# Performance work log

Measured on AMD Instinct MI355X. Metric: run time of the kernel, lower is better.

Reference implementation:

```python
import jax, jax.numpy as jnp
import numpy as np

B, S, D, H = 2, 2048, 1024, 16
DK = D // H


def setup_inputs() -> dict:
    key = jax.random.key(0)
    ks = jax.random.split(key, 7)
    q = jax.random.normal(ks[0], (B, S, D), dtype=jnp.float32)
    k = jax.random.normal(ks[1], (B, S, D), dtype=jnp.float32)
    v = jax.random.normal(ks[2], (B, S, D), dtype=jnp.float32)
    # causal mask: mask==0 positions get -1e9 before softmax
    mask = jnp.tril(jnp.ones((S, S), dtype=jnp.int32))[None, None, :, :]
    scale = 0.02
    w_q = jax.random.normal(ks[3], (D, D), dtype=jnp.float32) * scale
    w_k = jax.random.normal(ks[4], (D, D), dtype=jnp.float32) * scale
    w_v = jax.random.normal(ks[5], (D, D), dtype=jnp.float32) * scale
    w_o = jax.random.normal(ks[6], (D, D), dtype=jnp.float32) * scale
    return {"q": q, "k": k, "v": v, "mask": mask,
            "w_q": w_q, "w_k": w_k, "w_v": w_v, "w_o": w_o}


def reference(q, k, v, mask, w_q, w_k, w_v, w_o):
    # nn.Linear(bias=False): x @ W.T
    query = q @ w_q.T  # [B,S,D]
    key = k @ w_k.T
    value = v @ w_v.T
    # split heads -> [B,H,S,DK]
    query = query.reshape(B, S, H, DK).transpose(0, 2, 1, 3)
    key = key.reshape(B, S, H, DK).transpose(0, 2, 1, 3)
    value = value.reshape(B, S, H, DK).transpose(0, 2, 1, 3)
    scores = jnp.einsum('bhqd,bhkd->bhqk', query, key) / jnp.sqrt(
        jnp.asarray(DK, dtype=query.dtype))
    scores = jnp.where(mask == 0, jnp.asarray(-1e9, scores.dtype), scores)
    attn = jax.nn.softmax(scores, axis=-1)  # dropout p=0.0 -> identity
    x = jnp.einsum('bhqk,bhkd->bhqd', attn, value)  # [B,H,S,DK]
    x = x.transpose(0, 2, 1, 3).reshape(B, S, D)
    return x @ w_o.T
```

## Files before the change

kernel.cpp:

```cpp
#include <hip/hip_runtime.h>

typedef __attribute__((ext_vector_type(8))) short short8;
typedef __attribute__((ext_vector_type(4))) float f32x4;

#define DEVI static __device__ __forceinline__

constexpr int BB = 2, SS = 2048, DD = 1024, HH = 16, DKK = 64;
constexpr size_t QN = (size_t)BB * SS * DD;
constexpr size_t WN = (size_t)DD * DD;

constexpr size_t OFF_WQ = 3 * QN;
constexpr size_t OFF_WO = OFF_WQ + 3 * WN;
constexpr size_t OFF_QM = OFF_WQ + 4 * WN;
constexpr size_t OFF_KM = OFF_QM + QN;
constexpr size_t OFF_VM = OFF_QM + 2 * QN;
constexpr size_t OFF_XC = OFF_QM + 3 * QN;

DEVI unsigned short f2bf(float f) {
  unsigned int u = __float_as_uint(f);
  u = (u + 0x7fffu + ((u >> 16) & 1u)) >> 16;
  return (unsigned short)u;
}

DEVI f32x4 fzero() { f32x4 z = {0.f, 0.f, 0.f, 0.f}; return z; }

DEVI void gld16(const void* g, void* l) {
  __builtin_amdgcn_global_load_lds((__attribute__((address_space(1))) void*)g,
                                   (__attribute__((address_space(3))) void*)l,
                                   16, 0, 0);
}

DEVI short8 mk8u(unsigned int a, unsigned int b, unsigned int c, unsigned int d) {
  union { short8 s; unsigned int u[4]; } x;
  x.u[0] = a; x.u[1] = b; x.u[2] = c; x.u[3] = d;
  return x.s;
}

DEVI short8 mk8q(unsigned long long lo, unsigned long long hi) {
  union { short8 s; unsigned long long q[2]; } x;
  x.q[0] = lo; x.q[1] = hi;
  return x.s;
}

DEVI unsigned int pkbf(float a, float b) {
  return __builtin_amdgcn_perm(__float_as_uint(b), __float_as_uint(a), 0x07060302u);
}

#define VMBAR(N) asm volatile("s_waitcnt vmcnt(" #N ")\n\ts_barrier" ::: "memory")
#define LGKM0                                      \
  do {                                             \
    asm volatile("s_waitcnt lgkmcnt(0)" ::: "memory"); \
    __builtin_amdgcn_sched_barrier(0);             \
  } while (0)

__global__ __launch_bounds__(256) void convert_all(
    const float* __restrict__ q, const float* __restrict__ k,
    const float* __restrict__ v, const float* __restrict__ wq,
    const float* __restrict__ wk, const float* __restrict__ wv,
    const float* __restrict__ wo, unsigned short* __restrict__ ws) {
  size_t t = (size_t)blockIdx.x * 256 + threadIdx.x;
  size_t e = t * 4;
  const float* src;
  size_t base, idx;
  if (e < 3 * QN) {
    size_t a = e >> 22;
    idx = e & (QN - 1);
    src = (a == 0) ? q : (a == 1) ? k : v;
    base = a * QN;
  } else {
    size_t r = e - 3 * QN;
    size_t a = r >> 20;
    idx = r & (WN - 1);
    src = (a == 0) ? wq : (a == 1) ? wk : (a == 2) ? wv : wo;
    base = 3 * QN + a * WN;
  }
  float4 f = *(const float4*)(src + idx);
  ushort4 o;
  o.x = f2bf(f.x); o.y = f2bf(f.y); o.z = f2bf(f.z); o.w = f2bf(f.w);
  *(ushort4*)(ws + base + idx) = o;
}

__global__ __launch_bounds__(512, 2) void proj_gemm(unsigned short* __restrict__ ws) {
  __shared__ unsigned short lds[65536];
  const int tid = threadIdx.x;
  const int w = tid >> 6, l = tid & 63;
  const int lr = l & 15, qd = l >> 4, l7 = l & 7, l3 = l >> 3;
  const int wr = w >> 2, wc = w & 3;

  const int orig = blockIdx.x;
  const int swz = (orig & 7) * 24 + (orig >> 3);
  const int mt = swz >> 2, nt = swz & 3;
  const int z = mt >> 4;
  const int m0 = (mt & 15) * 256, n0 = nt * 256;

  const unsigned short* Ab = ws + (size_t)z * QN;
  const unsigned short* Wb = ws + OFF_WQ + (size_t)z * WN;
  unsigned short* O = ws + OFF_QM + (size_t)z * QN;

  f32x4 acc[8][4];
#pragma unroll
  for (int i = 0; i < 8; ++i)
#pragma unroll
    for (int j = 0; j < 4; ++j) acc[i][j] = fzero();

  auto stage = [&](int buf, int ab, int h, int kt) {
    const unsigned short* src = ab ? Wb : Ab;
    const int rc0 = (ab ? n0 : m0) + h * 128 + w * 8 + l3;
    const int kofs = kt * 64 + ((l7 ^ l3) * 8);
    unsigned short* d = &lds[buf * 32768 + ab * 16384 + h * 8192 + w * 512];
#pragma unroll
    for (int u = 0; u < 2; ++u)
      gld16(src + (size_t)(rc0 + u * 64) * DD + kofs, d + u * 4096);
  };
  auto rdA = [&](int buf, int fi, int ks) -> short8 {
    const int rg = (fi * 2 + wr) * 16 + lr;
    const int c2 = (ks * 4 + qd) ^ l7;
    return *(const short8*)&lds[buf * 32768 + rg * 64 + c2 * 8];
  };
  auto rdB = [&](int buf, int fj, int ks) -> short8 {
    const int rg = (fj * 4 + wc) * 16 + lr;
    const int c2 = (ks * 4 + qd) ^ l7;
    return *(const short8*)&lds[buf * 32768 + 16384 + rg * 64 + c2 * 8];
  };

  stage(0, 0, 0, 0);
  stage(0, 1, 0, 0);
  stage(0, 1, 1, 0);
  stage(0, 0, 1, 0);

  constexpr int NT = DD / 64;
#pragma unroll 1
  for (int t = 0; t < NT; ++t) {
    const int rb = t & 1, wb = rb ^ 1;
    const bool g = (t + 1 < NT);
    short8 af[4][2], bf[2][2], bh[2][2];

    VMBAR(4);
    if (g) stage(wb, 0, 0, t + 1);
#pragma unroll
    for (int mi = 0; mi < 4; ++mi)
#pragma unroll
      for (int ks = 0; ks < 2; ++ks) af[mi][ks] = rdA(rb, mi, ks);
#pragma unroll
    for (int nj = 0; nj < 2; ++nj)
#pragma unroll
      for (int ks = 0; ks < 2; ++ks) bf[nj][ks] = rdB(rb, nj, ks);
    LGKM0;
    __builtin_amdgcn_s_setprio(1);
#pragma unroll
    for (int mi = 0; mi < 4; ++mi)
#pragma unroll
      for (int nj = 0; nj < 2; ++nj)
#pragma unroll
        for (int ks = 0; ks < 2; ++ks)
          acc[mi][nj] = __builtin_amdgcn_mfma_f32_16x16x32_bf16(
              af[mi][ks], bf[nj][ks], acc[mi][nj], 0, 0, 0);
    __builtin_amdgcn_s_setprio(0);

    if (g) { VMBAR(4); } else { VMBAR(2); }
    if (g) stage(wb, 1, 0, t + 1);
#pragma unroll
    for (int nj = 0; nj < 2; ++nj)
#pragma unroll
      for (int ks = 0; ks < 2; ++ks) bh[nj][ks] = rdB(rb, 2 + nj, ks);
    LGKM0;
    __builtin_amdgcn_s_setprio(1);
#pragma unroll
    for (int mi = 0; mi < 4; ++mi)
#pragma unroll
      for (int nj = 0; nj < 2; ++nj)
#pragma unroll
        for (int ks = 0; ks < 2; ++ks)
          acc[mi][2 + nj] = __builtin_amdgcn_mfma_f32_16x16x32_bf16(
              af[mi][ks], bh[nj][ks], acc[mi][2 + nj], 0, 0, 0);
    __builtin_amdgcn_s_setprio(0);

    if (g) { VMBAR(4); } else { VMBAR(0); }
    if (g) stage(wb, 1, 1, t + 1);
#pragma unroll
    for (int mi = 0; mi < 4; ++mi)
#pragma unroll
      for (int ks = 0; ks < 2; ++ks) af[mi][ks] = rdA(rb, 4 + mi, ks);
    LGKM0;
    __builtin_amdgcn_s_setprio(1);
#pragma unroll
    for (int mi = 0; mi < 4; ++mi)
#pragma unroll
      for (int nj = 0; nj < 2; ++nj)
#pragma unroll
        for (int ks = 0; ks < 2; ++ks)
          acc[4 + mi][nj] = __builtin_amdgcn_mfma_f32_16x16x32_bf16(
              af[mi][ks], bf[nj][ks], acc[4 + mi][nj], 0, 0, 0);
    __builtin_amdgcn_s_setprio(0);

    if (g) stage(wb, 0, 1, t + 1);
    __builtin_amdgcn_s_setprio(1);
#pragma unroll
    for (int mi = 0; mi < 4; ++mi)
#pragma unroll
      for (int nj = 0; nj < 2; ++nj)
#pragma unroll
        for (int ks = 0; ks < 2; ++ks)
          acc[4 + mi][2 + nj] = __builtin_amdgcn_mfma_f32_16x16x32_bf16(
              af[mi][ks], bh[nj][ks], acc[4 + mi][2 + nj], 0, 0, 0);
    __builtin_amdgcn_s_setprio(0);
  }

  if (z == 2) {
#pragma unroll
    for (int fi = 0; fi < 8; ++fi)
#pragma unroll
      for (int fj = 0; fj < 4; ++fj) {
        const int n = n0 + (fj * 4 + wc) * 16 + lr;
        const int h = n >> 6, dk = n & 63;
        const int m = m0 + (fi * 2 + wr) * 16 + qd * 4;
        const int b = m >> 11, s = m & 2047;
        ushort4 pk;
        pk.x = f2bf(acc[fi][fj][0]); pk.y = f2bf(acc[fi][fj][1]);
        pk.z = f2bf(acc[fi][fj][2]); pk.w = f2bf(acc[fi][fj][3]);
        *(ushort4*)&O[((size_t)(b * HH + h) * DKK + dk) * SS + s] = pk;
      }
  } else {
#pragma unroll
    for (int fi = 0; fi < 8; ++fi)
#pragma unroll
      for (int fj = 0; fj < 4; ++fj) {
        const int n = n0 + (fj * 4 + wc) * 16 + lr;
        const int h = n >> 6, dk = n & 63;
#pragma unroll
        for (int i = 0; i < 4; ++i) {
          const int m = m0 + (fi * 2 + wr) * 16 + qd * 4 + i;
          const int b = m >> 11, s = m & 2047;
          O[((size_t)(b * HH + h) * SS + s) * DKK + dk] = f2bf(acc[fi][fj][i]);
        }
      }
  }
}

__global__ __launch_bounds__(256) void flash_attn(
    const unsigned short* __restrict__ Qm, const unsigned short* __restrict__ Km,
    const unsigned short* __restrict__ Vt, unsigned short* __restrict__ Xc) {
  __shared__ unsigned short Kl[2][4096];
  __shared__ unsigned short Vl[2][4096];
  const int head = blockIdx.x, qy = blockIdx.y, b = blockIdx.z;
  const int qt = (qy < 16) ? qy : 47 - qy;
  const int tid = threadIdx.x, w = tid >> 6, l = tid & 63, lr = l & 15, qd = l >> 4;
  const int slr = lr ^ ((lr >> 3) << 2);
  const size_t bh = (size_t)(b * HH + head);
  const unsigned short* Qb = Qm + bh * SS * DKK;
  const unsigned short* Kb = Km + bh * SS * DKK;
  const unsigned short* Vb = Vt + bh * DKK * SS;

  const int nkv = qt + 1;
  const int qrow = qt * 64 + w * 16 + lr;

  const int s0 = w, s1 = w + 4;
  const unsigned short* kb0 =
      &Kb[(size_t)((s0 >> 1) * 16 + lr) * DKK + (s0 & 1) * 32 + qd * 8];
  const unsigned short* kb1 =
      &Kb[(size_t)((s1 >> 1) * 16 + lr) * DKK + (s1 & 1) * 32 + qd * 8];
  const unsigned short* vb0 =
      &Vb[(size_t)((s0 >> 1) * 16 + slr) * SS + (s0 & 1) * 32 + qd * 8];
  const unsigned short* vb1 =
      &Vb[(size_t)((s1 >> 1) * 16 + slr) * SS + (s1 & 1) * 32 + qd * 8];

  const int loOff = ((qd >> 1) * 16 + slr) * 8 + (qd & 1) * 4;
  const int hiOff = ((2 + (qd >> 1)) * 16 + slr) * 8 + (qd & 1) * 4;

  short8 qf0 = *(const short8*)&Qb[(size_t)qrow * DKK + qd * 8];
  short8 qf1 = *(const short8*)&Qb[(size_t)qrow * DKK + 32 + qd * 8];

  f32x4 o[4];
#pragma unroll
  for (int i = 0; i < 4; ++i) o[i] = fzero();
  float ll = 0.f;
  const float c1 = 0.18033688011112042f;
  const float mc = 8.0f * c1;

  {
    gld16(kb0, &Kl[0][s0 * 512]);
    gld16(kb1, &Kl[0][s1 * 512]);
    gld16(vb0, &Vl[0][s0 * 512]);
    gld16(vb1, &Vl[0][s1 * 512]);
  }

#pragma unroll 1
  for (int kv = 0; kv < nkv; ++kv) {
    __syncthreads();
    const int cur = kv & 1;
    if (kv + 1 < nkv) {
      const size_t koff = (size_t)(kv + 1) * (64 * DKK);
      const size_t voff = (size_t)(kv + 1) * 64;
      gld16(kb0 + koff, &Kl[cur ^ 1][s0 * 512]);
      gld16(kb1 + koff, &Kl[cur ^ 1][s1 * 512]);
      gld16(vb0 + voff, &Vl[cur ^ 1][s0 * 512]);
      gld16(vb1 + voff, &Vl[cur ^ 1][s1 * 512]);
    }

    {
      const int kv0 = kv * 64;
      f32x4 sc[4];
#pragma unroll
      for (int nt = 0; nt < 4; ++nt) {
        short8 kf0 = *(const short8*)&Kl[cur][(nt * 2 + 0) * 512 + l * 8];
        short8 kf1 = *(const short8*)&Kl[cur][(nt * 2 + 1) * 512 + l * 8];
        f32x4 zz = fzero();
        zz = __builtin_amdgcn_mfma_f32_16x16x32_bf16(kf0, qf0, zz, 0, 0, 0);
        sc[nt] = __builtin_amdgcn_mfma_f32_16x16x32_bf16(kf1, qf1, zz, 0, 0, 0);
      }
      if (kv == qt) {
#pragma unroll
        for (int nt = 0; nt < 4; ++nt)
#pragma unroll
          for (int i = 0; i < 4; ++i) {
            const int kvi = kv0 + nt * 16 + qd * 4 + i;
            if (kvi > qrow) sc[nt][i] = -3e38f;
          }
      }

      float rs = 0.f;
#pragma unroll
      for (int nt = 0; nt < 4; ++nt)
#pragma unroll
        for (int i = 0; i < 4; ++i) {
          const float pp = exp2f(fmaf(sc[nt][i], c1, -mc));
          sc[nt][i] = pp;
          rs += pp;
        }
      rs += __shfl_xor(rs, 16);
      rs += __shfl_xor(rs, 32);
      ll += rs;

      unsigned int pd[4][2];
#pragma unroll
      for (int f = 0; f < 4; ++f) {
        pd[f][0] = pkbf(sc[f][0], sc[f][1]);
        pd[f][1] = pkbf(sc[f][2], sc[f][3]);
      }

#pragma unroll
      for (int kh = 0; kh < 2; ++kh) {
        short8 bfr = mk8u(pd[2 * kh][0], pd[2 * kh][1],
                          pd[2 * kh + 1][0], pd[2 * kh + 1][1]);
#pragma unroll
        for (int mt = 0; mt < 4; ++mt) {
          const int sbase = (mt * 2 + kh) * 512;
          const unsigned long long lo =
              *(const unsigned long long*)&Vl[cur][sbase + loOff];
          const unsigned long long hi =
              *(const unsigned long long*)&Vl[cur][sbase + hiOff];
          o[mt] = __builtin_amdgcn_mfma_f32_16x16x32_bf16(mk8q(lo, hi), bfr,
                                                          o[mt], 0, 0, 0);
        }
      }
    }
  }

  const float inv = 1.0f / ll;
  unsigned short* Xr = Xc + ((size_t)b * SS + qrow) * DD + (size_t)head * DKK;
#pragma unroll
  for (int mt = 0; mt < 4; ++mt)
#pragma unroll
    for (int i = 0; i < 4; ++i)
      Xr[mt * 16 + qd * 4 + i] = f2bf(o[mt][i] * inv);
}

__global__ __launch_bounds__(256, 2) void out_gemm(
    const unsigned short* __restrict__ Xc, const unsigned short* __restrict__ Wo,
    float* __restrict__ out) {
  __shared__ unsigned short lds[32768];
  const int tid = threadIdx.x;
  const int w = tid >> 6, l = tid & 63;
  const int lr = l & 15, qd = l >> 4, l7 = l & 7, l3 = l >> 3;
  const int wr = w >> 1, wc = w & 1;
  const int m0 = blockIdx.x * 128, n0 = blockIdx.y * 128;

  f32x4 acc[4][4];
#pragma unroll
  for (int i = 0; i < 4; ++i)
#pragma unroll
    for (int j = 0; j < 4; ++j) acc[i][j] = fzero();

  auto stage = [&](int buf, int ab, int h, int kt) {
    const unsigned short* src = ab ? Wo : Xc;
    const int rc0 = (ab ? n0 : m0) + h * 64 + w * 8 + l3;
    const int kofs = kt * 64 + ((l7 ^ l3) * 8);
    unsigned short* d = &lds[buf * 16384 + ab * 8192 + h * 4096 + w * 512];
#pragma unroll
    for (int u = 0; u < 2; ++u)
      gld16(src + (size_t)(rc0 + u * 32) * DD + kofs, d + u * 2048);
  };
  auto rdA = [&](int buf, int mf, int ks) -> short8 {
    const int rg = mf * 16 + lr;
    const int c2 = (ks * 4 + qd) ^ l7;
    return *(const short8*)&lds[buf * 16384 + rg * 64 + c2 * 8];
  };
  auto rdB = [&](int buf, int nf, int ks) -> short8 {
    const int rg = nf * 16 + lr;
    const int c2 = (ks * 4 + qd) ^ l7;
    return *(const short8*)&lds[buf * 16384 + 8192 + rg * 64 + c2 * 8];
  };

  stage(0, 0, 0, 0);
  stage(0, 1, 0, 0);
  stage(0, 1, 1, 0);
  stage(0, 0, 1, 0);

  constexpr int NT = DD / 64;
#pragma unroll 1
  for (int t = 0; t < NT; ++t) {
    const int rb = t & 1, wb = rb ^ 1;
    const bool g = (t + 1 < NT);
    short8 af[2][2], bf[2][2], bh[2][2];

    VMBAR(4);
    if (g) stage(wb, 0, 0, t + 1);
#pragma unroll
    for (int mi = 0; mi < 2; ++mi)
#pragma unroll
      for (int ks = 0; ks < 2; ++ks) af[mi][ks] = rdA(rb, mi * 2 + wr, ks);
#pragma unroll
    for (int nj = 0; nj < 2; ++nj)
#pragma unroll
      for (int ks = 0; ks < 2; ++ks) bf[nj][ks] = rdB(rb, nj * 2 + wc, ks);
    LGKM0;
    __builtin_amdgcn_s_setprio(1);
#pragma unroll
    for (int mi = 0; mi < 2; ++mi)
#pragma unroll
      for (int nj = 0; nj < 2; ++nj)
#pragma unroll
        for (int ks = 0; ks < 2; ++ks)
          acc[mi][nj] = __builtin_amdgcn_mfma_f32_16x16x32_bf16(
              af[mi][ks], bf[nj][ks], acc[mi][nj], 0, 0, 0);
    __builtin_amdgcn_s_setprio(0);

    if (g) { VMBAR(4); } else { VMBAR(2); }
    if (g) stage(wb, 1, 0, t + 1);
#pragma unroll
    for (int nj = 0; nj < 2; ++nj)
#pragma unroll
      for (int ks = 0; ks < 2; ++ks) bh[nj][ks] = rdB(rb, (2 + nj) * 2 + wc, ks);
    LGKM0;
    __builtin_amdgcn_s_setprio(1);
#pragma unroll
    for (int mi = 0; mi < 2; ++mi)
#pragma unroll
      for (int nj = 0; nj < 2; ++nj)
#pragma unroll
        for (int ks = 0; ks < 2; ++ks)
          acc[mi][2 + nj] = __builtin_amdgcn_mfma_f32_16x16x32_bf16(
              af[mi][ks], bh[nj][ks], acc[mi][2 + nj], 0, 0, 0);
    __builtin_amdgcn_s_setprio(0);

    if (g) { VMBAR(4); } else { VMBAR(0); }
    if (g) stage(wb, 1, 1, t + 1);
#pragma unroll
    for (int mi = 0; mi < 2; ++mi)
#pragma unroll
      for (int ks = 0; ks < 2; ++ks) af[mi][ks] = rdA(rb, (2 + mi) * 2 + wr, ks);
    LGKM0;
    __builtin_amdgcn_s_setprio(1);
#pragma unroll
    for (int mi = 0; mi < 2; ++mi)
#pragma unroll
      for (int nj = 0; nj < 2; ++nj)
#pragma unroll
        for (int ks = 0; ks < 2; ++ks)
          acc[2 + mi][nj] = __builtin_amdgcn_mfma_f32_16x16x32_bf16(
              af[mi][ks], bf[nj][ks], acc[2 + mi][nj], 0, 0, 0);
    __builtin_amdgcn_s_setprio(0);

    if (g) stage(wb, 0, 1, t + 1);
    __builtin_amdgcn_s_setprio(1);
#pragma unroll
    for (int mi = 0; mi < 2; ++mi)
#pragma unroll
      for (int nj = 0; nj < 2; ++nj)
#pragma unroll
        for (int ks = 0; ks < 2; ++ks)
          acc[2 + mi][2 + nj] = __builtin_amdgcn_mfma_f32_16x16x32_bf16(
              af[mi][ks], bh[nj][ks], acc[2 + mi][2 + nj], 0, 0, 0);
    __builtin_amdgcn_s_setprio(0);
  }

#pragma unroll
  for (int a = 0; a < 4; ++a)
#pragma unroll
    for (int c = 0; c < 4; ++c) {
      const int n = n0 + (c * 2 + wc) * 16 + lr;
#pragma unroll
      for (int i = 0; i < 4; ++i) {
        const int m = m0 + (a * 2 + wr) * 16 + qd * 4 + i;
        out[(size_t)m * DD + n] = acc[a][c][i];
      }
    }
}

extern "C" void kernel_launch(void* const* d_in, const int* in_sizes, int n_in,
                              void* d_out, int out_size, void* d_ws, size_t ws_size,
                              hipStream_t stream) {
  (void)in_sizes; (void)n_in; (void)out_size; (void)ws_size;
  const float* q  = (const float*)d_in[0];
  const float* k  = (const float*)d_in[1];
  const float* v  = (const float*)d_in[2];
  const float* wq = (const float*)d_in[4];
  const float* wk = (const float*)d_in[5];
  const float* wv = (const float*)d_in[6];
  const float* wo = (const float*)d_in[7];
  unsigned short* ws = (unsigned short*)d_ws;
  float* out = (float*)d_out;

  convert_all<<<dim3(16384), dim3(256), 0, stream>>>(q, k, v, wq, wk, wv, wo, ws);
  proj_gemm<<<dim3(192), dim3(512), 0, stream>>>(ws);
  flash_attn<<<dim3(16, 32, 2), dim3(256), 0, stream>>>(ws + OFF_QM, ws + OFF_KM,
                                                        ws + OFF_VM, ws + OFF_XC);
  out_gemm<<<dim3(32, 8), dim3(256), 0, stream>>>(ws + OFF_XC, ws + OFF_WO, out);
}
```

Before: 227.6 us.

## Pair heavy and light causal query tiles in one 512-thread attention block

```diff
diff --git a/kernel.cpp b/kernel.cpp
--- a/kernel.cpp
+++ b/kernel.cpp
@@ -237,13 +237,13 @@
   }
 }
 
-__global__ __launch_bounds__(256) void flash_attn(
+__global__ __launch_bounds__(512) void flash_attn(
     const unsigned short* __restrict__ Qm, const unsigned short* __restrict__ Km,
     const unsigned short* __restrict__ Vt, unsigned short* __restrict__ Xc) {
   __shared__ unsigned short Kl[2][4096];
   __shared__ unsigned short Vl[2][4096];
-  const int head = blockIdx.x, qy = blockIdx.y, b = blockIdx.z;
-  const int qt = (qy < 16) ? qy : 47 - qy;
+  const int head = blockIdx.x, py = blockIdx.y, b = blockIdx.z;
+  const int p = b ? 15 - py : py;
   const int tid = threadIdx.x, w = tid >> 6, l = tid & 63, lr = l & 15, qd = l >> 4;
   const int slr = lr ^ ((lr >> 3) << 2);
   const size_t bh = (size_t)(b * HH + head);
@@ -251,19 +251,13 @@
   const unsigned short* Kb = Km + bh * SS * DKK;
   const unsigned short* Vb = Vt + bh * DKK * SS;
 
-  const int nkv = qt + 1;
-  const int qrow = qt * 64 + w * 16 + lr;
-
-  const int s0 = w, s1 = w + 4;
-  const unsigned short* kb0 =
-      &Kb[(size_t)((s0 >> 1) * 16 + lr) * DKK + (s0 & 1) * 32 + qd * 8];
-  const unsigned short* kb1 =
-      &Kb[(size_t)((s1 >> 1) * 16 + lr) * DKK + (s1 & 1) * 32 + qd * 8];
-  const unsigned short* vb0 =
-      &Vb[(size_t)((s0 >> 1) * 16 + slr) * SS + (s0 & 1) * 32 + qd * 8];
-  const unsigned short* vb1 =
-      &Vb[(size_t)((s1 >> 1) * 16 + slr) * SS + (s1 & 1) * 32 + qd * 8];
-
+  const bool heavy = (w < 4);
+  const int qt = heavy ? (31 - p) : p;
+  const int nkv = 32 - p;
+  const int qrow = qt * 64 + (w & 3) * 16 + lr;
+
+  const int s0 = heavy ? w : (w - 4);
+  const int s1 = s0 + 4;
   const int loOff = ((qd >> 1) * 16 + slr) * 8 + (qd & 1) * 4;
   const int hiOff = ((2 + (qd >> 1)) * 16 + slr) * 8 + (qd & 1) * 4;
 
@@ -278,10 +272,17 @@
   const float mc = 8.0f * c1;
 
   {
-    gld16(kb0, &Kl[0][s0 * 512]);
-    gld16(kb1, &Kl[0][s1 * 512]);
-    gld16(vb0, &Vl[0][s0 * 512]);
-    gld16(vb1, &Vl[0][s1 * 512]);
+    if (heavy) {
+      gld16(&Kb[(size_t)((s0 >> 1) * 16 + lr) * DKK + (s0 & 1) * 32 + qd * 8],
+            &Kl[0][s0 * 512]);
+      gld16(&Kb[(size_t)((s1 >> 1) * 16 + lr) * DKK + (s1 & 1) * 32 + qd * 8],
+            &Kl[0][s1 * 512]);
+    } else {
+      gld16(&Vb[(size_t)((s0 >> 1) * 16 + slr) * SS + (s0 & 1) * 32 + qd * 8],
+            &Vl[0][s0 * 512]);
+      gld16(&Vb[(size_t)((s1 >> 1) * 16 + slr) * SS + (s1 & 1) * 32 + qd * 8],
+            &Vl[0][s1 * 512]);
+    }
   }
 
 #pragma unroll 1
@@ -289,15 +290,21 @@
     __syncthreads();
     const int cur = kv & 1;
     if (kv + 1 < nkv) {
-      const size_t koff = (size_t)(kv + 1) * (64 * DKK);
-      const size_t voff = (size_t)(kv + 1) * 64;
-      gld16(kb0 + koff, &Kl[cur ^ 1][s0 * 512]);
-      gld16(kb1 + koff, &Kl[cur ^ 1][s1 * 512]);
-      gld16(vb0 + voff, &Vl[cur ^ 1][s0 * 512]);
-      gld16(vb1 + voff, &Vl[cur ^ 1][s1 * 512]);
+      const int kv0n = (kv + 1) * 64;
+      if (heavy) {
+        gld16(&Kb[(size_t)(kv0n + (s0 >> 1) * 16 + lr) * DKK + (s0 & 1) * 32 + qd * 8],
+              &Kl[cur ^ 1][s0 * 512]);
+        gld16(&Kb[(size_t)(kv0n + (s1 >> 1) * 16 + lr) * DKK + (s1 & 1) * 32 + qd * 8],
+              &Kl[cur ^ 1][s1 * 512]);
+      } else {
+        gld16(&Vb[(size_t)((s0 >> 1) * 16 + slr) * SS + kv0n + (s0 & 1) * 32 + qd * 8],
+              &Vl[cur ^ 1][s0 * 512]);
+        gld16(&Vb[(size_t)((s1 >> 1) * 16 + slr) * SS + kv0n + (s1 & 1) * 32 + qd * 8],
+              &Vl[cur ^ 1][s1 * 512]);
+      }
     }
 
-    {
+    if (kv <= qt) {
       const int kv0 = kv * 64;
       f32x4 sc[4];
 #pragma unroll
@@ -318,18 +325,14 @@
           }
       }
 
-      float rs = 0.f;
 #pragma unroll
       for (int nt = 0; nt < 4; ++nt)
 #pragma unroll
         for (int i = 0; i < 4; ++i) {
           const float pp = exp2f(fmaf(sc[nt][i], c1, -mc));
           sc[nt][i] = pp;
-          rs += pp;
+          ll += pp;
         }
-      rs += __shfl_xor(rs, 16);
-      rs += __shfl_xor(rs, 32);
-      ll += rs;
 
       unsigned int pd[4][2];
 #pragma unroll
@@ -355,6 +358,9 @@
       }
     }
   }
+
+  ll += __shfl_xor(ll, 16);
+  ll += __shfl_xor(ll, 32);
 
   const float inv = 1.0f / ll;
   unsigned short* Xr = Xc + ((size_t)b * SS + qrow) * DD + (size_t)head * DKK;
@@ -513,7 +519,7 @@
 
   convert_all<<<dim3(16384), dim3(256), 0, stream>>>(q, k, v, wq, wk, wv, wo, ws);
   proj_gemm<<<dim3(192), dim3(512), 0, stream>>>(ws);
-  flash_attn<<<dim3(16, 32, 2), dim3(256), 0, stream>>>(ws + OFF_QM, ws + OFF_KM,
+  flash_attn<<<dim3(16, 16, 2), dim3(512), 0, stream>>>(ws + OFF_QM, ws + OFF_KM,
                                                         ws + OFF_VM, ws + OFF_XC);
   out_gemm<<<dim3(32, 8), dim3(256), 0, stream>>>(ws + OFF_XC, ws + OFF_WO, out);
 }
```

After: 215.6 us. 5.3% less time.
